# Performance work log

Hardware: AMD Instinct MI355X
Metric: run time of the kernel (lower is better)

## Reference

```python
import jax, jax.numpy as jnp
import numpy as np

B, T, N = 2, 512, 512
H = 64          # hidden_dim
S = 8           # static_dim
C = 8           # coord_dim
DYN = 4         # dynamic feature dim (hard-coded in module)
SELF_LOOP_W = 1.0


def setup_inputs() -> dict:
    key = jax.random.key(0)
    ks = jax.random.split(key, 12)
    x = jax.random.normal(ks[0], (B, T, N), dtype=jnp.float32)
    mask = jax.random.randint(ks[1], (B, T, N), 0, 2).astype(jnp.float32)
    static_context = jax.random.normal(ks[2], (N, S), dtype=jnp.float32)
    node_coords = jax.random.normal(ks[3], (N, C), dtype=jnp.float32)
    sc = 0.1
    W1 = jax.random.normal(ks[4], (DYN + S, H), dtype=jnp.float32) * sc
    b1 = jnp.zeros((H,), dtype=jnp.float32)
    W2 = jax.random.normal(ks[5], (H, H), dtype=jnp.float32) * sc
    b2 = jnp.zeros((H,), dtype=jnp.float32)
    W3 = jax.random.normal(ks[6], (4 * H, H), dtype=jnp.float32) * sc
    b3 = jnp.zeros((H,), dtype=jnp.float32)
    W4 = jax.random.normal(ks[7], (H, 1), dtype=jnp.float32) * sc
    b4 = jnp.zeros((1,), dtype=jnp.float32)
    return {"x": x, "mask": mask, "static_context": static_context,
            "node_coords": node_coords, "W1": W1, "b1": b1, "W2": W2,
            "b2": b2, "W3": W3, "b3": b3, "W4": W4, "b4": b4}


def _dynamic_context(x, mask):
    observed = 1.0 - mask                                  # (B,T,N)
    count = jnp.maximum(observed.sum(axis=1), 1.0)          # (B,N)
    mean = (x * observed).sum(axis=1) / count               # (B,N)
    centered = (x - mean[:, None, :]) * observed
    std = jnp.sqrt((centered ** 2).sum(axis=1) / count + 1e-6)
    # last observed value per node
    t_idx = jnp.arange(x.shape[1], dtype=x.dtype)[None, :, None]
    latest = jnp.argmax(t_idx * observed, axis=1)           # (B,N) int
    last = jnp.take_along_axis(x, latest[:, None, :], axis=1)[:, 0, :]
    missing_ratio = mask.mean(axis=1)                       # (B,N)
    return jnp.stack([mean, std, last, missing_ratio], axis=-1)  # (B,N,4)


def _prior_adjacency(node_coords):
    diff = node_coords[:, None, :] - node_coords[None, :, :]  # (N,N,C)
    d2 = (diff ** 2).sum(-1)
    dist = jnp.where(d2 > 0, jnp.sqrt(jnp.where(d2 > 0, d2, 1.0)), 0.0)
    prior = 1.0 / (1.0 + dist)
    eye = jnp.eye(node_coords.shape[0], dtype=node_coords.dtype)
    return prior * (1.0 - eye)


def reference(x, mask, static_context, node_coords, W1, b1, W2, b2, W3, b3, W4, b4):
    batch = x.shape[0]
    node_dynamic = _dynamic_context(x, mask)                         # (B,N,4)
    node_static = jnp.broadcast_to(static_context[None], (batch,) + static_context.shape)
    feats = jnp.concatenate([node_dynamic, node_static], axis=-1)    # (B,N,4+S)
    h = jax.nn.relu(feats @ W1 + b1)
    node_repr = jax.nn.relu(h @ W2 + b2)                              # (B,N,H)

    h_i = node_repr[:, :, None, :]                                    # (B,N,1,H)
    h_j = node_repr[:, None, :, :]                                    # (B,1,N,H)
    hi = jnp.broadcast_to(h_i, (batch, N, N, H))
    hj = jnp.broadcast_to(h_j, (batch, N, N, H))
    pair = jnp.concatenate([hi, hj, jnp.abs(hi - hj), hi * hj], axis=-1)  # (B,N,N,4H)
    e = jax.nn.relu(pair @ W3 + b3)
    edge_mod = jax.nn.relu((e @ W4 + b4)[..., 0])                     # (B,N,N)

    prior = _prior_adjacency(node_coords)[None]                       # (1,N,N)
    eye = jnp.eye(N, dtype=x.dtype)[None]
    adapt = edge_mod * prior + eye * SELF_LOOP_W
    degree = jnp.maximum(adapt.sum(axis=-1), 1e-6)                    # (B,N)
    inv_sqrt = degree ** -0.5
    return inv_sqrt[:, :, None] * adapt * inv_sqrt[:, None, :]
```

## Files before the change

### kernel.cpp

```cpp
#include <hip/hip_runtime.h>
#include <hip/hip_bf16.h>
#include <math.h>

#define B_ 2
#define T_ 512
#define N_ 512
#define H_ 64

typedef __attribute__((ext_vector_type(8))) short short8;
typedef __attribute__((ext_vector_type(4))) float floatx4;

__device__ inline short f2bf(float f) {
    union { float f; unsigned u; } v; v.f = f;
    unsigned r = (v.u + 0x7fffu + ((v.u >> 16) & 1u)) >> 16;
    return (short)r;
}

__global__ void prep_kernel(const float* __restrict__ coords, const float* __restrict__ W3,
                            float* __restrict__ prior, short* __restrict__ W3p) {
    int idx = blockIdx.x * 256 + threadIdx.x;
    if (blockIdx.x < 1024) {
        int i = idx >> 9, j = idx & (N_ - 1);
        float d2 = 0.f;
#pragma unroll
        for (int c = 0; c < 8; c++) {
            float df = coords[i * 8 + c] - coords[j * 8 + c];
            d2 += df * df;
        }
        float dist = (d2 > 0.f) ? sqrtf(d2) : 0.f;
        prior[idx] = (i == j) ? 0.f : 1.f / (1.f + dist);
    } else {
        int k = idx - 1024 * 256;
        int t = k & 7;
        int l = (k >> 3) & 63;
        int f = k >> 9;
        int s = f >> 2, nt = f & 3;
        int quad = l >> 4, col = l & 15;
        W3p[k] = f2bf(W3[(128 + s * 32 + quad * 8 + t) * H_ + nt * 16 + col]);
    }
}

__global__ void dyn_part_kernel(const float* __restrict__ x, const float* __restrict__ mask,
                                float* __restrict__ part) {
    int blk = blockIdx.x;
    int b  = blk >> 8;
    int nc = (blk >> 5) & 7;
    int tc = blk & 31;
    int tn = threadIdx.x & 63;
    int tt = threadIdx.x >> 6;
    int n  = nc * 64 + tn;

    float sx = 0.f, sxx = 0.f, cnt = 0.f, msum = 0.f, bv = 0.f, bt = -1.f;
#pragma unroll
    for (int it = 0; it < 4; it++) {
        int t = tc * 16 + it * 4 + tt;
        int off = (b * T_ + t) * N_ + n;
        float xv = x[off];
        float mv = mask[off];
        float obs = 1.f - mv;
        sx   += xv * obs;
        sxx  += xv * xv * obs;
        cnt  += obs;
        msum += mv;
        if (obs > 0.5f) { bt = (float)t; bv = xv; }
    }

    __shared__ float red[6][4][64];
    red[0][tt][tn] = sx;  red[1][tt][tn] = sxx; red[2][tt][tn] = cnt;
    red[3][tt][tn] = msum; red[4][tt][tn] = bv; red[5][tt][tn] = bt;
    __syncthreads();

    if (threadIdx.x < 64) {
        float Sx = 0.f, Sxx = 0.f, Cnt = 0.f, Ms = 0.f, Bv = 0.f, Bt = -1.f;
#pragma unroll
        for (int u = 0; u < 4; u++) {
            Sx  += red[0][u][tn];
            Sxx += red[1][u][tn];
            Cnt += red[2][u][tn];
            Ms  += red[3][u][tn];
            float btu = red[5][u][tn];
            if (btu > Bt) { Bt = btu; Bv = red[4][u][tn]; }
        }
        const int plane = B_ * 32 * N_;
        int base = (b * 32 + tc) * N_ + n;
        part[0 * plane + base] = Sx;
        part[1 * plane + base] = Sxx;
        part[2 * plane + base] = Cnt;
        part[3 * plane + base] = Ms;
        part[4 * plane + base] = Bv;
        part[5 * plane + base] = Bt;
    }
}

__global__ void dyn_red_kernel(const float* __restrict__ part, const float* __restrict__ x,
                               float* __restrict__ dyn) {
    int u = blockIdx.x * 256 + threadIdx.x;
    int b = u >> 9, n = u & (N_ - 1);
    const int plane = B_ * 32 * N_;
    float Sx = 0.f, Sxx = 0.f, Cnt = 0.f, Ms = 0.f, Bv = 0.f, Bt = -1.f;
    for (int tc = 0; tc < 32; tc++) {
        int base = (b * 32 + tc) * N_ + n;
        Sx  += part[0 * plane + base];
        Sxx += part[1 * plane + base];
        Cnt += part[2 * plane + base];
        Ms  += part[3 * plane + base];
        float bt = part[5 * plane + base];
        if (bt > Bt) { Bt = bt; Bv = part[4 * plane + base]; }
    }
    float count = fmaxf(Cnt, 1.f);
    float mean  = Sx / count;
    float var   = (Sxx - 2.f * mean * Sx + mean * mean * Cnt) / count;
    float stdv  = sqrtf(fmaxf(var, 0.f) + 1e-6f);
    float last  = (Bt >= 0.f) ? Bv : x[b * T_ * N_ + n];
    float mr    = Ms * (1.f / (float)T_);
    dyn[u * 4 + 0] = mean;
    dyn[u * 4 + 1] = stdv;
    dyn[u * 4 + 2] = last;
    dyn[u * 4 + 3] = mr;
}

__global__ __launch_bounds__(64) void mlp_kernel(
        const float* __restrict__ dyn, const float* __restrict__ sc,
        const float* __restrict__ W1, const float* __restrict__ b1,
        const float* __restrict__ W2, const float* __restrict__ b2,
        const float* __restrict__ W3,
        float* __restrict__ nr, float* __restrict__ P, float* __restrict__ Qp) {
    int blk = blockIdx.x;
    int b = blk >> 9;
    int n = blk & (N_ - 1);
    int o = threadIdx.x;

    __shared__ float f[12];
    __shared__ float h[H_];
    __shared__ float r[H_];

    if (o < 4)        f[o] = dyn[(b * N_ + n) * 4 + o];
    else if (o < 12)  f[o] = sc[n * 8 + (o - 4)];
    __syncthreads();

    float a = b1[o];
#pragma unroll
    for (int k = 0; k < 12; k++) a += f[k] * W1[k * H_ + o];
    h[o] = fmaxf(a, 0.f);
    __syncthreads();

    float a2 = b2[o];
#pragma unroll 8
    for (int k = 0; k < H_; k++) a2 += h[k] * W2[k * H_ + o];
    float rv = fmaxf(a2, 0.f);
    r[o] = rv;
    nr[(b * N_ + n) * H_ + o] = rv;
    __syncthreads();

    float p = 0.f, q = 0.f;
#pragma unroll 8
    for (int k = 0; k < H_; k++) {
        float rk = r[k];
        p += rk * W3[k * H_ + o];
        q += rk * W3[(H_ + k) * H_ + o];
    }
    P[(b * N_ + n) * H_ + o] = p;
    Qp[(b * N_ + n) * H_ + (o & 15) * 4 + (o >> 4)] = q;
}

__global__ __launch_bounds__(256) void pair_mfma_kernel(
        const float* __restrict__ nr, const float* __restrict__ P,
        const float* __restrict__ Qp, const short* __restrict__ W3p,
        const float* __restrict__ b3, const float* __restrict__ W4,
        const float* __restrict__ b4, const float* __restrict__ prior,
        float* __restrict__ adapt, float* __restrict__ degree) {
    int blk = blockIdx.x;
    int b = blk >> 9;
    int i = blk & (N_ - 1);
    int tid = threadIdx.x;
    int w = tid >> 6;
    int l = tid & 63;
    int col = l & 15;
    int quad = l >> 4;

    short8 bf[4][4];
#pragma unroll
    for (int s = 0; s < 4; s++)
#pragma unroll
        for (int nt = 0; nt < 4; nt++)
            bf[s][nt] = *(const short8*)(W3p + (((s * 4 + nt) * 64 + l) << 3));

    const float* hi_row = nr + (b * N_ + i) * H_;
    floatx4 hiA0 = *(const floatx4*)(hi_row + quad * 8);
    floatx4 hiA1 = *(const floatx4*)(hi_row + quad * 8 + 4);
    floatx4 hiB0 = *(const floatx4*)(hi_row + 32 + quad * 8);
    floatx4 hiB1 = *(const floatx4*)(hi_row + 32 + quad * 8 + 4);

    float pb3[4], w4v[4];
#pragma unroll
    for (int nt = 0; nt < 4; nt++) {
        int o = nt * 16 + col;
        pb3[nt] = P[(b * N_ + i) * H_ + o] + b3[o];
        w4v[nt] = W4[o];
    }
    float b4s = b4[0];
    const float* prow = prior + i * N_;
    float rsum = 0.f;

    for (int mt = 0; mt < 8; mt++) {
        int j0 = w * 128 + mt * 16;

        const float* hj_row = nr + (b * N_ + j0 + col) * H_;
        floatx4 hjA0 = *(const floatx4*)(hj_row + quad * 8);
        floatx4 hjA1 = *(const floatx4*)(hj_row + quad * 8 + 4);
        floatx4 hjB0 = *(const floatx4*)(hj_row + 32 + quad * 8);
        floatx4 hjB1 = *(const floatx4*)(hj_row + 32 + quad * 8 + 4);

        union { short8 s; __hip_bfloat162 h[4]; } a0, a1, a2, a3;
#pragma unroll
        for (int t = 0; t < 2; t++) {
            a0.h[t]     = __float22bfloat162_rn(make_float2(fabsf(hiA0[2*t] - hjA0[2*t]),
                                                            fabsf(hiA0[2*t+1] - hjA0[2*t+1])));
            a0.h[t + 2] = __float22bfloat162_rn(make_float2(fabsf(hiA1[2*t] - hjA1[2*t]),
                                                            fabsf(hiA1[2*t+1] - hjA1[2*t+1])));
            a1.h[t]     = __float22bfloat162_rn(make_float2(fabsf(hiB0[2*t] - hjB0[2*t]),
                                                            fabsf(hiB0[2*t+1] - hjB0[2*t+1])));
            a1.h[t + 2] = __float22bfloat162_rn(make_float2(fabsf(hiB1[2*t] - hjB1[2*t]),
                                                            fabsf(hiB1[2*t+1] - hjB1[2*t+1])));
            a2.h[t]     = __float22bfloat162_rn(make_float2(hiA0[2*t] * hjA0[2*t],
                                                            hiA0[2*t+1] * hjA0[2*t+1]));
            a2.h[t + 2] = __float22bfloat162_rn(make_float2(hiA1[2*t] * hjA1[2*t],
                                                            hiA1[2*t+1] * hjA1[2*t+1]));
            a3.h[t]     = __float22bfloat162_rn(make_float2(hiB0[2*t] * hjB0[2*t],
                                                            hiB0[2*t+1] * hjB0[2*t+1]));
            a3.h[t + 2] = __float22bfloat162_rn(make_float2(hiB1[2*t] * hjB1[2*t],
                                                            hiB1[2*t+1] * hjB1[2*t+1]));
        }

        floatx4 acc[4];
#pragma unroll
        for (int nt = 0; nt < 4; nt++) acc[nt] = (floatx4){0.f, 0.f, 0.f, 0.f};
#pragma unroll
        for (int nt = 0; nt < 4; nt++) {
            acc[nt] = __builtin_amdgcn_mfma_f32_16x16x32_bf16(a0.s, bf[0][nt], acc[nt], 0, 0, 0);
            acc[nt] = __builtin_amdgcn_mfma_f32_16x16x32_bf16(a1.s, bf[1][nt], acc[nt], 0, 0, 0);
            acc[nt] = __builtin_amdgcn_mfma_f32_16x16x32_bf16(a2.s, bf[2][nt], acc[nt], 0, 0, 0);
            acc[nt] = __builtin_amdgcn_mfma_f32_16x16x32_bf16(a3.s, bf[3][nt], acc[nt], 0, 0, 0);
        }

        floatx4 pv = *(const floatx4*)(prow + j0 + quad * 4);
        float ed[4];
#pragma unroll
        for (int r = 0; r < 4; r++) {
            int j = j0 + quad * 4 + r;
            floatx4 qv = *(const floatx4*)(Qp + (b * N_ + j) * H_ + col * 4);
            float p = 0.f;
#pragma unroll
            for (int nt = 0; nt < 4; nt++)
                p += fmaxf(acc[nt][r] + pb3[nt] + qv[nt], 0.f) * w4v[nt];
            p += __shfl_xor(p, 1);
            p += __shfl_xor(p, 2);
            p += __shfl_xor(p, 4);
            p += __shfl_xor(p, 8);
            float edge = fmaxf(p + b4s, 0.f);
            float ad = (j == i) ? 1.0f : edge * pv[r];
            ed[r] = ad;
            rsum += ad;
        }
        if (col == 0) {
            *(floatx4*)&adapt[(size_t)(b * N_ + i) * N_ + j0 + quad * 4] =
                (floatx4){ed[0], ed[1], ed[2], ed[3]};
        }
    }

    rsum += __shfl_xor(rsum, 16);
    rsum += __shfl_xor(rsum, 32);
    __shared__ float sRow[4];
    if (l == 0) sRow[w] = rsum;
    __syncthreads();
    if (tid == 0) degree[b * N_ + i] = sRow[0] + sRow[1] + sRow[2] + sRow[3];
}

__global__ void norm_kernel(const float* __restrict__ adapt, const float* __restrict__ deg,
                            float* __restrict__ out) {
    int idx = blockIdx.x * 256 + threadIdx.x;
    int b = idx >> 16;
    int r = (idx >> 7) & (N_ - 1);
    int c4 = (idx & 127) << 2;
    float dr = rsqrtf(fmaxf(deg[b * N_ + r], 1e-6f));
    floatx4 a = *(const floatx4*)(adapt + ((size_t)idx << 2));
    floatx4 o;
#pragma unroll
    for (int k = 0; k < 4; k++)
        o[k] = dr * a[k] * rsqrtf(fmaxf(deg[b * N_ + c4 + k], 1e-6f));
    *(floatx4*)(out + ((size_t)idx << 2)) = o;
}

extern "C" void kernel_launch(void* const* d_in, const int* in_sizes, int n_in,
                              void* d_out, int out_size, void* d_ws, size_t ws_size,
                              hipStream_t stream) {
    const float* x      = (const float*)d_in[0];
    const float* mask   = (const float*)d_in[1];
    const float* sc     = (const float*)d_in[2];
    const float* coords = (const float*)d_in[3];
    const float* W1 = (const float*)d_in[4];
    const float* b1 = (const float*)d_in[5];
    const float* W2 = (const float*)d_in[6];
    const float* b2 = (const float*)d_in[7];
    const float* W3 = (const float*)d_in[8];
    const float* b3 = (const float*)d_in[9];
    const float* W4 = (const float*)d_in[10];
    const float* b4 = (const float*)d_in[11];
    float* out = (float*)d_out;

    float* w = (float*)d_ws;
    float* dyn   = w;
    float* nr    = w + 4096;
    float* P     = w + 69632;
    float* Qp    = w + 135168;
    float* adapt = w + 200704;
    float* deg   = w + 724992;
    float* prior = w + 726016;
    short* W3p   = (short*)(w + 988160);
    float* part  = adapt;

    prep_kernel<<<1056, 256, 0, stream>>>(coords, W3, prior, W3p);
    dyn_part_kernel<<<512, 256, 0, stream>>>(x, mask, part);
    dyn_red_kernel<<<4, 256, 0, stream>>>(part, x, dyn);
    mlp_kernel<<<B_ * N_, 64, 0, stream>>>(dyn, sc, W1, b1, W2, b2, W3, nr, P, Qp);
    pair_mfma_kernel<<<B_ * N_, 256, 0, stream>>>(nr, P, Qp, W3p, b3, W4, b4, prior, adapt, deg);
    norm_kernel<<<512, 256, 0, stream>>>(adapt, deg, out);
}
```

Before: 132.4 us.

## Fuse dynamic stats into prep and node kernels, prefetch h_j rows in pair loop

The partial time-reduction moves into the prep kernel as extra blocks, so it runs alongside the prior and W3 packing. The final reduction is folded into the node MLP kernel with a wavefront shuffle reduction, which drops two launches and the dyn buffer. In the pair MFMA kernel, the next tile's h_j rows, the prior and the Qp loads are issued early (software prefetch with a fully unrolled loop) to hide global latency. In exchange, each node block now redundantly reads 32 partials per node, and register pressure rises.

After: 119.2 us. -10.0%, faster.

```diff
diff --git a/kernel.cpp b/kernel.cpp
--- a/kernel.cpp
+++ b/kernel.cpp
@@ -16,10 +16,61 @@
     return (short)r;
 }
 
-__global__ void prep_kernel(const float* __restrict__ coords, const float* __restrict__ W3,
-                            float* __restrict__ prior, short* __restrict__ W3p) {
-    int idx = blockIdx.x * 256 + threadIdx.x;
-    if (blockIdx.x < 1024) {
+__global__ void prep_kernel(const float* __restrict__ x, const float* __restrict__ mask,
+                            const float* __restrict__ coords, const float* __restrict__ W3,
+                            float* __restrict__ part, float* __restrict__ prior,
+                            short* __restrict__ W3p) {
+    int blk = blockIdx.x;
+    if (blk < 512) {
+        int b  = blk >> 8;
+        int nc = (blk >> 5) & 7;
+        int tc = blk & 31;
+        int tn = threadIdx.x & 63;
+        int tt = threadIdx.x >> 6;
+        int n  = nc * 64 + tn;
+
+        float sx = 0.f, sxx = 0.f, cnt = 0.f, msum = 0.f, bv = 0.f, bt = -1.f;
+#pragma unroll
+        for (int it = 0; it < 4; it++) {
+            int t = tc * 16 + it * 4 + tt;
+            int off = (b * T_ + t) * N_ + n;
+            float xv = x[off];
+            float mv = mask[off];
+            float obs = 1.f - mv;
+            sx   += xv * obs;
+            sxx  += xv * xv * obs;
+            cnt  += obs;
+            msum += mv;
+            if (obs > 0.5f) { bt = (float)t; bv = xv; }
+        }
+
+        __shared__ float red[6][4][64];
+        red[0][tt][tn] = sx;  red[1][tt][tn] = sxx; red[2][tt][tn] = cnt;
+        red[3][tt][tn] = msum; red[4][tt][tn] = bv; red[5][tt][tn] = bt;
+        __syncthreads();
+
+        if (threadIdx.x < 64) {
+            float Sx = 0.f, Sxx = 0.f, Cnt = 0.f, Ms = 0.f, Bv = 0.f, Bt = -1.f;
+#pragma unroll
+            for (int u = 0; u < 4; u++) {
+                Sx  += red[0][u][tn];
+                Sxx += red[1][u][tn];
+                Cnt += red[2][u][tn];
+                Ms  += red[3][u][tn];
+                float btu = red[5][u][tn];
+                if (btu > Bt) { Bt = btu; Bv = red[4][u][tn]; }
+            }
+            const int plane = B_ * 32 * N_;
+            int base = (b * 32 + tc) * N_ + n;
+            part[0 * plane + base] = Sx;
+            part[1 * plane + base] = Sxx;
+            part[2 * plane + base] = Cnt;
+            part[3 * plane + base] = Ms;
+            part[4 * plane + base] = Bv;
+            part[5 * plane + base] = Bt;
+        }
+    } else if (blk < 1536) {
+        int idx = (blk - 512) * 256 + threadIdx.x;
         int i = idx >> 9, j = idx & (N_ - 1);
         float d2 = 0.f;
 #pragma unroll
@@ -30,7 +81,7 @@
         float dist = (d2 > 0.f) ? sqrtf(d2) : 0.f;
         prior[idx] = (i == j) ? 0.f : 1.f / (1.f + dist);
     } else {
-        int k = idx - 1024 * 256;
+        int k = (blk - 1536) * 256 + threadIdx.x;
         int t = k & 7;
         int l = (k >> 3) & 63;
         int f = k >> 9;
@@ -40,87 +91,9 @@
     }
 }
 
-__global__ void dyn_part_kernel(const float* __restrict__ x, const float* __restrict__ mask,
-                                float* __restrict__ part) {
-    int blk = blockIdx.x;
-    int b  = blk >> 8;
-    int nc = (blk >> 5) & 7;
-    int tc = blk & 31;
-    int tn = threadIdx.x & 63;
-    int tt = threadIdx.x >> 6;
-    int n  = nc * 64 + tn;
-
-    float sx = 0.f, sxx = 0.f, cnt = 0.f, msum = 0.f, bv = 0.f, bt = -1.f;
-#pragma unroll
-    for (int it = 0; it < 4; it++) {
-        int t = tc * 16 + it * 4 + tt;
-        int off = (b * T_ + t) * N_ + n;
-        float xv = x[off];
-        float mv = mask[off];
-        float obs = 1.f - mv;
-        sx   += xv * obs;
-        sxx  += xv * xv * obs;
-        cnt  += obs;
-        msum += mv;
-        if (obs > 0.5f) { bt = (float)t; bv = xv; }
-    }
-
-    __shared__ float red[6][4][64];
-    red[0][tt][tn] = sx;  red[1][tt][tn] = sxx; red[2][tt][tn] = cnt;
-    red[3][tt][tn] = msum; red[4][tt][tn] = bv; red[5][tt][tn] = bt;
-    __syncthreads();
-
-    if (threadIdx.x < 64) {
-        float Sx = 0.f, Sxx = 0.f, Cnt = 0.f, Ms = 0.f, Bv = 0.f, Bt = -1.f;
-#pragma unroll
-        for (int u = 0; u < 4; u++) {
-            Sx  += red[0][u][tn];
-            Sxx += red[1][u][tn];
-            Cnt += red[2][u][tn];
-            Ms  += red[3][u][tn];
-            float btu = red[5][u][tn];
-            if (btu > Bt) { Bt = btu; Bv = red[4][u][tn]; }
-        }
-        const int plane = B_ * 32 * N_;
-        int base = (b * 32 + tc) * N_ + n;
-        part[0 * plane + base] = Sx;
-        part[1 * plane + base] = Sxx;
-        part[2 * plane + base] = Cnt;
-        part[3 * plane + base] = Ms;
-        part[4 * plane + base] = Bv;
-        part[5 * plane + base] = Bt;
-    }
-}
-
-__global__ void dyn_red_kernel(const float* __restrict__ part, const float* __restrict__ x,
-                               float* __restrict__ dyn) {
-    int u = blockIdx.x * 256 + threadIdx.x;
-    int b = u >> 9, n = u & (N_ - 1);
-    const int plane = B_ * 32 * N_;
-    float Sx = 0.f, Sxx = 0.f, Cnt = 0.f, Ms = 0.f, Bv = 0.f, Bt = -1.f;
-    for (int tc = 0; tc < 32; tc++) {
-        int base = (b * 32 + tc) * N_ + n;
-        Sx  += part[0 * plane + base];
-        Sxx += part[1 * plane + base];
-        Cnt += part[2 * plane + base];
-        Ms  += part[3 * plane + base];
-        float bt = part[5 * plane + base];
-        if (bt > Bt) { Bt = bt; Bv = part[4 * plane + base]; }
-    }
-    float count = fmaxf(Cnt, 1.f);
-    float mean  = Sx / count;
-    float var   = (Sxx - 2.f * mean * Sx + mean * mean * Cnt) / count;
-    float stdv  = sqrtf(fmaxf(var, 0.f) + 1e-6f);
-    float last  = (Bt >= 0.f) ? Bv : x[b * T_ * N_ + n];
-    float mr    = Ms * (1.f / (float)T_);
-    dyn[u * 4 + 0] = mean;
-    dyn[u * 4 + 1] = stdv;
-    dyn[u * 4 + 2] = last;
-    dyn[u * 4 + 3] = mr;
-}
-
-__global__ __launch_bounds__(64) void mlp_kernel(
-        const float* __restrict__ dyn, const float* __restrict__ sc,
+__global__ __launch_bounds__(64) void node_kernel(
+        const float* __restrict__ part, const float* __restrict__ x,
+        const float* __restrict__ sc,
         const float* __restrict__ W1, const float* __restrict__ b1,
         const float* __restrict__ W2, const float* __restrict__ b2,
         const float* __restrict__ W3,
@@ -134,8 +107,38 @@
     __shared__ float h[H_];
     __shared__ float r[H_];
 
-    if (o < 4)        f[o] = dyn[(b * N_ + n) * 4 + o];
-    else if (o < 12)  f[o] = sc[n * 8 + (o - 4)];
+    {
+        const int plane = B_ * 32 * N_;
+        float Sx = 0.f, Sxx = 0.f, Cnt = 0.f, Ms = 0.f, Bv = 0.f, Bt = -1.f;
+        if (o < 32) {
+            int base = (b * 32 + o) * N_ + n;
+            Sx  = part[0 * plane + base];
+            Sxx = part[1 * plane + base];
+            Cnt = part[2 * plane + base];
+            Ms  = part[3 * plane + base];
+            Bv  = part[4 * plane + base];
+            Bt  = part[5 * plane + base];
+        }
+#pragma unroll
+        for (int off = 1; off < 32; off <<= 1) {
+            Sx  += __shfl_xor(Sx, off);
+            Sxx += __shfl_xor(Sxx, off);
+            Cnt += __shfl_xor(Cnt, off);
+            Ms  += __shfl_xor(Ms, off);
+            float obt = __shfl_xor(Bt, off);
+            float obv = __shfl_xor(Bv, off);
+            if (obt > Bt) { Bt = obt; Bv = obv; }
+        }
+        if (o == 0) {
+            float count = fmaxf(Cnt, 1.f);
+            float mean  = Sx / count;
+            float var   = (Sxx - 2.f * mean * Sx + mean * mean * Cnt) / count;
+            float stdv  = sqrtf(fmaxf(var, 0.f) + 1e-6f);
+            float last  = (Bt >= 0.f) ? Bv : x[b * T_ * N_ + n];
+            f[0] = mean; f[1] = stdv; f[2] = last; f[3] = Ms * (1.f / (float)T_);
+        }
+        if (o >= 4 && o < 12) f[o] = sc[n * 8 + (o - 4)];
+    }
     __syncthreads();
 
     float a = b1[o];
@@ -200,36 +203,56 @@
     }
     float b4s = b4[0];
     const float* prow = prior + i * N_;
+    const float* nrb = nr + (b * N_) * H_;
     float rsum = 0.f;
 
+    floatx4 hA0, hA1, hB0, hB1;
+    {
+        const float* p0 = nrb + (w * 128 + col) * H_;
+        hA0 = *(const floatx4*)(p0 + quad * 8);
+        hA1 = *(const floatx4*)(p0 + quad * 8 + 4);
+        hB0 = *(const floatx4*)(p0 + 32 + quad * 8);
+        hB1 = *(const floatx4*)(p0 + 32 + quad * 8 + 4);
+    }
+
+#pragma unroll
     for (int mt = 0; mt < 8; mt++) {
         int j0 = w * 128 + mt * 16;
 
-        const float* hj_row = nr + (b * N_ + j0 + col) * H_;
-        floatx4 hjA0 = *(const floatx4*)(hj_row + quad * 8);
-        floatx4 hjA1 = *(const floatx4*)(hj_row + quad * 8 + 4);
-        floatx4 hjB0 = *(const floatx4*)(hj_row + 32 + quad * 8);
-        floatx4 hjB1 = *(const floatx4*)(hj_row + 32 + quad * 8 + 4);
+        floatx4 nA0, nA1, nB0, nB1;
+        if (mt < 7) {
+            const float* pn = nrb + (j0 + 16 + col) * H_;
+            nA0 = *(const floatx4*)(pn + quad * 8);
+            nA1 = *(const floatx4*)(pn + quad * 8 + 4);
+            nB0 = *(const floatx4*)(pn + 32 + quad * 8);
+            nB1 = *(const floatx4*)(pn + 32 + quad * 8 + 4);
+        }
+
+        floatx4 pv = *(const floatx4*)(prow + j0 + quad * 4);
+        floatx4 qv[4];
+#pragma unroll
+        for (int r = 0; r < 4; r++)
+            qv[r] = *(const floatx4*)(Qp + (b * N_ + j0 + quad * 4 + r) * H_ + col * 4);
 
         union { short8 s; __hip_bfloat162 h[4]; } a0, a1, a2, a3;
 #pragma unroll
         for (int t = 0; t < 2; t++) {
-            a0.h[t]     = __float22bfloat162_rn(make_float2(fabsf(hiA0[2*t] - hjA0[2*t]),
-                                                            fabsf(hiA0[2*t+1] - hjA0[2*t+1])));
-            a0.h[t + 2] = __float22bfloat162_rn(make_float2(fabsf(hiA1[2*t] - hjA1[2*t]),
-                                                            fabsf(hiA1[2*t+1] - hjA1[2*t+1])));
-            a1.h[t]     = __float22bfloat162_rn(make_float2(fabsf(hiB0[2*t] - hjB0[2*t]),
-                                                            fabsf(hiB0[2*t+1] - hjB0[2*t+1])));
-            a1.h[t + 2] = __float22bfloat162_rn(make_float2(fabsf(hiB1[2*t] - hjB1[2*t]),
-                                                            fabsf(hiB1[2*t+1] - hjB1[2*t+1])));
-            a2.h[t]     = __float22bfloat162_rn(make_float2(hiA0[2*t] * hjA0[2*t],
-                                                            hiA0[2*t+1] * hjA0[2*t+1]));
-            a2.h[t + 2] = __float22bfloat162_rn(make_float2(hiA1[2*t] * hjA1[2*t],
-                                                            hiA1[2*t+1] * hjA1[2*t+1]));
-            a3.h[t]     = __float22bfloat162_rn(make_float2(hiB0[2*t] * hjB0[2*t],
-                                                            hiB0[2*t+1] * hjB0[2*t+1]));
-            a3.h[t + 2] = __float22bfloat162_rn(make_float2(hiB1[2*t] * hjB1[2*t],
-                                                            hiB1[2*t+1] * hjB1[2*t+1]));
+            a0.h[t]     = __float22bfloat162_rn(make_float2(fabsf(hiA0[2*t] - hA0[2*t]),
+                                                            fabsf(hiA0[2*t+1] - hA0[2*t+1])));
+            a0.h[t + 2] = __float22bfloat162_rn(make_float2(fabsf(hiA1[2*t] - hA1[2*t]),
+                                                            fabsf(hiA1[2*t+1] - hA1[2*t+1])));
+            a1.h[t]     = __float22bfloat162_rn(make_float2(fabsf(hiB0[2*t] - hB0[2*t]),
+                                                            fabsf(hiB0[2*t+1] - hB0[2*t+1])));
+            a1.h[t + 2] = __float22bfloat162_rn(make_float2(fabsf(hiB1[2*t] - hB1[2*t]),
+                                                            fabsf(hiB1[2*t+1] - hB1[2*t+1])));
+            a2.h[t]     = __float22bfloat162_rn(make_float2(hiA0[2*t] * hA0[2*t],
+                                                            hiA0[2*t+1] * hA0[2*t+1]));
+            a2.h[t + 2] = __float22bfloat162_rn(make_float2(hiA1[2*t] * hA1[2*t],
+                                                            hiA1[2*t+1] * hA1[2*t+1]));
+            a3.h[t]     = __float22bfloat162_rn(make_float2(hiB0[2*t] * hB0[2*t],
+                                                            hiB0[2*t+1] * hB0[2*t+1]));
+            a3.h[t + 2] = __float22bfloat162_rn(make_float2(hiB1[2*t] * hB1[2*t],
+                                                            hiB1[2*t+1] * hB1[2*t+1]));
         }
 
         floatx4 acc[4];
@@ -243,16 +266,14 @@
             acc[nt] = __builtin_amdgcn_mfma_f32_16x16x32_bf16(a3.s, bf[3][nt], acc[nt], 0, 0, 0);
         }
 
-        floatx4 pv = *(const floatx4*)(prow + j0 + quad * 4);
         float ed[4];
 #pragma unroll
         for (int r = 0; r < 4; r++) {
             int j = j0 + quad * 4 + r;
-            floatx4 qv = *(const floatx4*)(Qp + (b * N_ + j) * H_ + col * 4);
             float p = 0.f;
 #pragma unroll
             for (int nt = 0; nt < 4; nt++)
-                p += fmaxf(acc[nt][r] + pb3[nt] + qv[nt], 0.f) * w4v[nt];
+                p += fmaxf(acc[nt][r] + pb3[nt] + qv[r][nt], 0.f) * w4v[nt];
             p += __shfl_xor(p, 1);
             p += __shfl_xor(p, 2);
             p += __shfl_xor(p, 4);
@@ -266,6 +287,8 @@
             *(floatx4*)&adapt[(size_t)(b * N_ + i) * N_ + j0 + quad * 4] =
                 (floatx4){ed[0], ed[1], ed[2], ed[3]};
         }
+
+        if (mt < 7) { hA0 = nA0; hA1 = nA1; hB0 = nB0; hB1 = nB1; }
     }
 
     rsum += __shfl_xor(rsum, 16);
@@ -308,21 +331,18 @@
     const float* b4 = (const float*)d_in[11];
     float* out = (float*)d_out;
 
-    float* w = (float*)d_ws;
-    float* dyn   = w;
-    float* nr    = w + 4096;
-    float* P     = w + 69632;
-    float* Qp    = w + 135168;
-    float* adapt = w + 200704;
-    float* deg   = w + 724992;
-    float* prior = w + 726016;
-    short* W3p   = (short*)(w + 988160);
+    float* wsp = (float*)d_ws;
+    float* nr    = wsp;
+    float* P     = wsp + 65536;
+    float* Qp    = wsp + 131072;
+    float* prior = wsp + 196608;
+    short* W3p   = (short*)(wsp + 458752);
+    float* deg   = wsp + 462848;
+    float* adapt = wsp + 463872;
     float* part  = adapt;
 
-    prep_kernel<<<1056, 256, 0, stream>>>(coords, W3, prior, W3p);
-    dyn_part_kernel<<<512, 256, 0, stream>>>(x, mask, part);
-    dyn_red_kernel<<<4, 256, 0, stream>>>(part, x, dyn);
-    mlp_kernel<<<B_ * N_, 64, 0, stream>>>(dyn, sc, W1, b1, W2, b2, W3, nr, P, Qp);
+    prep_kernel<<<1568, 256, 0, stream>>>(x, mask, coords, W3, part, prior, W3p);
+    node_kernel<<<B_ * N_, 64, 0, stream>>>(part, x, sc, W1, b1, W2, b2, W3, nr, P, Qp);
     pair_mfma_kernel<<<B_ * N_, 256, 0, stream>>>(nr, P, Qp, W3p, b3, W4, b4, prior, adapt, deg);
     norm_kernel<<<512, 256, 0, stream>>>(adapt, deg, out);
 }
```
